# Kernel tuning notes

Hardware: AMD Instinct MI355X
Metric: run time of the kernel (lower is better)

The kernel has to match this reference:

```python
import jax, jax.numpy as jnp
import numpy as np

V = 32000   # vocab
D = 1024    # dim
H = 16      # query heads
HKV = 8     # kv heads (GQA)
DH = D // H # head dim = 64
L = 2       # layers
FF = 3584   # expert hidden dim
E = 8       # experts
K = 2       # top-k
EPS = 1e-5
BASE = 1000000.0
B, S = 1, 2048


def setup_inputs() -> dict:
    key = jax.random.key(0)
    ks = jax.random.split(key, 10)
    s = 0.02
    return {
        "x": jax.random.randint(ks[0], (B, S), 0, V, dtype=jnp.int64) if jax.config.jax_enable_x64 else jax.random.randint(ks[0], (B, S), 0, V),
        "emb": jax.random.normal(ks[1], (V, D), jnp.float32) * s,
        "ln_w": jnp.ones((L, D), jnp.float32),
        "ffln_w": jnp.ones((L, D), jnp.float32),
        "wq": jax.random.normal(ks[2], (L, D, H * DH), jnp.float32) * s,
        "wk": jax.random.normal(ks[3], (L, D, HKV * DH), jnp.float32) * s,
        "wv": jax.random.normal(ks[4], (L, D, HKV * DH), jnp.float32) * s,
        "wo": jax.random.normal(ks[5], (L, H * DH, D), jnp.float32) * s,
        "gate_w": jax.random.normal(ks[6], (L, E, D), jnp.float32) * s,
        "w1": jax.random.normal(ks[7], (L, E, FF, D), jnp.float32) * s,
        "w2": jax.random.normal(ks[8], (L, E, D, FF), jnp.float32) * s,
        "w3": jax.random.normal(ks[9], (L, E, FF, D), jnp.float32) * s,
        "dec_norm_w": jnp.ones((D,), jnp.float32),
    }


def rmsnorm(x, w):
    # LayerNormParameterized(use_mean=False, shift=False) == RMSNorm, pow in fp32
    xf = x.astype(jnp.float32)
    var = jnp.mean(xf * xf, axis=-1, keepdims=True)
    return ((xf * jax.lax.rsqrt(var + EPS)).astype(x.dtype)) * w


def rope(xh, pos):
    # interleaved (complex-pair) rotary embedding, xh: [B, S, h, DH]
    half = DH // 2
    freqs = 1.0 / (BASE ** (jnp.arange(0, half, dtype=jnp.float32) * 2.0 / DH))
    ang = pos[:, None] * freqs[None, :]                       # [S, half]
    cos = jnp.cos(ang)[None, :, None, :]
    sin = jnp.sin(ang)[None, :, None, :]
    x1 = xh[..., 0::2]
    x2 = xh[..., 1::2]
    out = jnp.stack([x1 * cos - x2 * sin, x1 * sin + x2 * cos], axis=-1)
    return out.reshape(xh.shape)


def reference(x, emb, ln_w, ffln_w, wq, wk, wv, wo, gate_w, w1, w2, w3, dec_norm_w):
    h = emb[x]                                                # [B, S, D]
    pos = jnp.arange(S, dtype=jnp.float32)
    causal = jnp.tril(jnp.ones((S, S), bool))[None, None]     # [1,1,S,S]
    scale = 1.0 / np.sqrt(DH).astype(np.float32)
    for i in range(L):
        # --- attention sub-layer ---
        res = h
        xn = rmsnorm(h, ln_w[i])
        q = rope((xn @ wq[i]).reshape(B, S, H, DH), pos)
        k = rope((xn @ wk[i]).reshape(B, S, HKV, DH), pos)
        v = (xn @ wv[i]).reshape(B, S, HKV, DH)
        rep = H // HKV
        k = jnp.repeat(k, rep, axis=2)                        # [B,S,H,DH]
        v = jnp.repeat(v, rep, axis=2)
        scores = jnp.einsum('bqhd,bkhd->bhqk', q, k) * scale
        scores = jnp.where(causal, scores, jnp.float32(-1e9))
        att = jax.nn.softmax(scores, axis=-1)
        o = jnp.einsum('bhqk,bkhd->bqhd', att, v).reshape(B, S, H * DH) @ wo[i]
        h = res + o
        # --- MoE FFN sub-layer ---
        res = h
        xn = rmsnorm(h, ffln_w[i]).reshape(B * S, D)          # [T, D]
        logits = xn @ gate_w[i].T                             # [T, E]
        gates = jax.nn.softmax(logits, axis=-1)
        topw, topi = jax.lax.top_k(gates, K)                  # [T, K]
        topw = topw / jnp.sum(topw, axis=-1, keepdims=True)
        # dense combine weights [T, E] (zero for unselected experts)
        cw = jnp.einsum('tk,tke->te', topw, jax.nn.one_hot(topi, E, dtype=topw.dtype))
        y = jnp.zeros_like(xn)
        for e in range(E):                                    # fixed small expert loop
            ye = (jax.nn.silu(xn @ w1[i, e].T) * (xn @ w3[i, e].T)) @ w2[i, e].T
            y = y + cw[:, e:e + 1] * ye
        h = res + y.reshape(B, S, D)
    return rmsnorm(h, dec_norm_w)
```

## Files before the change

### kernel.cpp

```cpp
#include <hip/hip_runtime.h>

using u16 = unsigned short;
using u32 = unsigned int;

#define TT 2048
#define DM 1024
#define NH 16
#define NKV 8
#define DHD 64
#define FFD 3584
#define NE 8

typedef __bf16 bf16x8 __attribute__((ext_vector_type(8)));
typedef float f32x4 __attribute__((ext_vector_type(4)));

__device__ __forceinline__ u16 f2bf(float x){
  return __builtin_bit_cast(u16, (__bf16)x);
}
__device__ __forceinline__ float bf2f(u16 h){
  return (float)__builtin_bit_cast(__bf16, h);
}
__device__ __forceinline__ f32x4 mfma16(bf16x8 a, bf16x8 b, f32x4 c){
  return __builtin_amdgcn_mfma_f32_16x16x32_bf16(a, b, c, 0, 0, 0);
}
__device__ __forceinline__ uint4 packhi8v(float4 a, float4 b){
  u16 h0=f2bf(a.x),h1=f2bf(a.y),h2=f2bf(a.z),h3=f2bf(a.w);
  u16 h4=f2bf(b.x),h5=f2bf(b.y),h6=f2bf(b.z),h7=f2bf(b.w);
  return make_uint4((u32)h0|((u32)h1<<16),(u32)h2|((u32)h3<<16),
                    (u32)h4|((u32)h5<<16),(u32)h6|((u32)h7<<16));
}
__device__ __forceinline__ uint4 packlo8v(float4 a, float4 b){
  u16 l0=f2bf(a.x-bf2f(f2bf(a.x))),l1=f2bf(a.y-bf2f(f2bf(a.y)));
  u16 l2=f2bf(a.z-bf2f(f2bf(a.z))),l3=f2bf(a.w-bf2f(f2bf(a.w)));
  u16 l4=f2bf(b.x-bf2f(f2bf(b.x))),l5=f2bf(b.y-bf2f(f2bf(b.y)));
  u16 l6=f2bf(b.z-bf2f(f2bf(b.z))),l7=f2bf(b.w-bf2f(f2bf(b.w)));
  return make_uint4((u32)l0|((u32)l1<<16),(u32)l2|((u32)l3<<16),
                    (u32)l4|((u32)l5<<16),(u32)l6|((u32)l7<<16));
}

#define SWZR(r) ((((r)>>1) ^ ((r)>>3)) & 3)
#define SWC(r,c) ((((c) ^ SWZR(r))) * 8)

__device__ __forceinline__ void glds16(const u16* g, u16* l){
  __builtin_amdgcn_global_load_lds(
      (const __attribute__((address_space(1))) void*)g,
      (__attribute__((address_space(3))) void*)l,
      16, 0, 0);
}

__global__ __launch_bounds__(256) void k_embed(const int* __restrict__ x,
    const float* __restrict__ emb, float* __restrict__ h){
  int t = blockIdx.x;
  int d = threadIdx.x * 4;
  float4 v = *reinterpret_cast<const float4*>(emb + (size_t)x[t] * DM + d);
  *reinterpret_cast<float4*>(h + (size_t)t * DM + d) = v;
}

template<int OUTF32>
__global__ __launch_bounds__(256) void k_rmsnorm(const float* __restrict__ in,
    const float* __restrict__ w, u16* __restrict__ oh, u16* __restrict__ ol,
    float* __restrict__ of){
  int t = blockIdx.x;
  int d4 = threadIdx.x * 4;
  float4 xv = *reinterpret_cast<const float4*>(in + (size_t)t * DM + d4);
  float ss = xv.x*xv.x + xv.y*xv.y + xv.z*xv.z + xv.w*xv.w;
#pragma unroll
  for (int m = 1; m < 64; m <<= 1) ss += __shfl_xor(ss, m);
  __shared__ float sred[4];
  if ((threadIdx.x & 63) == 0) sred[threadIdx.x >> 6] = ss;
  __syncthreads();
  float tot = sred[0] + sred[1] + sred[2] + sred[3];
  float r = 1.0f / sqrtf(tot * (1.0f / DM) + 1e-5f);
  float vv[4] = {xv.x, xv.y, xv.z, xv.w};
#pragma unroll
  for (int jj = 0; jj < 4; jj++){
    float xn = (vv[jj] * r) * w[d4 + jj];
    size_t a = (size_t)t * DM + d4 + jj;
    if constexpr (OUTF32){
      of[a] = xn;
    } else {
      u16 hi = f2bf(xn);
      oh[a] = hi;
      ol[a] = f2bf(xn - bf2f(hi));
    }
  }
}

template<int NHD>
__global__ __launch_bounds__(256) void k_rope(const float* __restrict__ in,
    u16* __restrict__ oh, u16* __restrict__ ol){
  int idx = blockIdx.x * 256 + threadIdx.x;
  int j = idx & 31;
  int hd = (idx >> 5) % NHD;
  int s = idx / (32 * NHD);
  size_t base = ((size_t)s * NHD + hd) * 64 + 2 * j;
  float x1 = in[base], x2 = in[base + 1];
  float xe = (float)j * 0.03125f;
  float yf = (float)pow(1.0e6, (double)xe);
  float fr = 1.0f / yf;
  float ang = (float)s * fr;
  double ad = (double)ang;
  float c  = (float)cos(ad);
  float sn = (float)sin(ad);
  float o1 = x1 * c - x2 * sn;
  float o2 = x1 * sn + x2 * c;
  u16 h1 = f2bf(o1), h2 = f2bf(o2);
  oh[base]     = h1; ol[base]     = f2bf(o1 - bf2f(h1));
  oh[base + 1] = h2; ol[base + 1] = f2bf(o2 - bf2f(h2));
}

__global__ __launch_bounds__(256) void k_splitbuf(const float* __restrict__ in,
    u16* __restrict__ oh, u16* __restrict__ ol, int n){
  int i = blockIdx.x * 256 + threadIdx.x;
  if (i < n){
    float x = in[i];
    u16 hi = f2bf(x);
    oh[i] = hi;
    ol[i] = f2bf(x - bf2f(hi));
  }
}

__global__ __launch_bounds__(256) void k_gate(const u16* __restrict__ xh,
    const u16* __restrict__ xl, const float* __restrict__ gw,
    int* __restrict__ topi, float* __restrict__ topw, int* __restrict__ cnt){
  int wv = threadIdx.x >> 6, lane = threadIdx.x & 63;
  int t = blockIdx.x * 4 + wv;
  float x[16];
#pragma unroll
  for (int i = 0; i < 16; i++){
    size_t a = (size_t)t * DM + lane + 64 * i;
    x[i] = bf2f(xh[a]) + bf2f(xl[a]);
  }
  float lgt[8];
#pragma unroll
  for (int e = 0; e < 8; e++){
    float s = 0.f;
#pragma unroll
    for (int i = 0; i < 16; i++) s += x[i] * gw[(size_t)e * DM + lane + 64 * i];
#pragma unroll
    for (int m = 1; m < 64; m <<= 1) s += __shfl_xor(s, m);
    lgt[e] = s;
  }
  float mx = lgt[0];
#pragma unroll
  for (int e = 1; e < 8; e++) mx = fmaxf(mx, lgt[e]);
  float p[8]; float sum = 0.f;
#pragma unroll
  for (int e = 0; e < 8; e++){ p[e] = expf(lgt[e] - mx); sum += p[e]; }
  float g[8];
#pragma unroll
  for (int e = 0; e < 8; e++) g[e] = p[e] / sum;
  int t0 = 0; float b0 = g[0];
#pragma unroll
  for (int e = 1; e < 8; e++) if (g[e] > b0){ b0 = g[e]; t0 = e; }
  int t1 = -1; float b1 = -1.f;
#pragma unroll
  for (int e = 0; e < 8; e++) if (e != t0 && g[e] > b1){ b1 = g[e]; t1 = e; }
  float ssum = b0 + b1;
  float w0 = b0 / ssum, w1 = b1 / ssum;
  if (lane == 0 && t < TT){
    topi[2*t] = t0; topi[2*t+1] = t1;
    topw[2*t] = w0; topw[2*t+1] = w1;
    atomicAdd(&cnt[t0], 1);
    atomicAdd(&cnt[t1], 1);
  }
}

__global__ void k_zero8(int* cnt){ if (threadIdx.x < 8) cnt[threadIdx.x] = 0; }

__global__ void k_scan(const int* __restrict__ cnt, int* __restrict__ offp, int* __restrict__ cur){
  if (threadIdx.x == 0){
    int r = 0;
    for (int e = 0; e < 8; e++){ offp[e] = r; r += cnt[e]; }
  }
  if (threadIdx.x < 8) cur[threadIdx.x] = 0;
}

__global__ __launch_bounds__(256) void k_scatter(const int* __restrict__ topi,
    const float* __restrict__ topw, const int* __restrict__ offp, int* __restrict__ cur,
    int* __restrict__ ftok, float* __restrict__ fwt){
  int t = blockIdx.x * 256 + threadIdx.x;
  if (t < TT){
#pragma unroll
    for (int j = 0; j < 2; j++){
      int e = topi[2*t + j];
      int p = atomicAdd(&cur[e], 1);
      ftok[offp[e] + p] = t;
      fwt[offp[e] + p] = topw[2*t + j];
    }
  }
}

#define GLDSA(BUF, KK) do { \
    glds16(Ah + gaA0 + (KK), (u16*)&Ash[BUF][awr0][0]); \
    glds16(Ah + gaA1 + (KK), (u16*)&Ash[BUF][awr1][0]); \
    if constexpr (SPLIT){ \
      glds16(Al + gaA0 + (KK), (u16*)&Asl[BUF][awr0][0]); \
      glds16(Al + gaA1 + (KK), (u16*)&Asl[BUF][awr1][0]); \
    } \
  } while(0)

#define GPRELOADB(KK) do { \
    if constexpr (BLAYOUT == 0){ \
      const float* bp_ = Bw + (size_t)(n0 + br0) * K + (KK) + cb8; \
      pB0 = *reinterpret_cast<const float4*>(bp_); \
      pB1 = *reinterpret_cast<const float4*>(bp_ + 4); \
      if constexpr (TN == 128){ \
        const float* bp2_ = Bw + (size_t)(n0 + br1) * K + (KK) + cb8; \
        pB2 = *reinterpret_cast<const float4*>(bp2_); \
        pB3 = *reinterpret_cast<const float4*>(bp2_ + 4); \
      } \
      if constexpr (DUAL){ \
        const float* bq_ = B3w + (size_t)(n0 + br0) * K + (KK) + cb8; \
        pB2 = *reinterpret_cast<const float4*>(bq_); \
        pB3 = *reinterpret_cast<const float4*>(bq_ + 4); \
      } \
    } else { \
      pB0 = *reinterpret_cast<const float4*>(Bw + (size_t)((KK) + kk1) * Nq + n0 + nn1); \
      pB1 = *reinterpret_cast<const float4*>(Bw + (size_t)((KK) + 16 + kk1) * Nq + n0 + nn1); \
    } \
  } while(0)

#define GSTOREB() do { \
    if constexpr (BLAYOUT == 0){ \
      *reinterpret_cast<uint4*>(&Bh1[br0][swB0]) = packhi8v(pB0, pB1); \
      if constexpr (SPLIT) *reinterpret_cast<uint4*>(&Bl1[br0][swB0]) = packlo8v(pB0, pB1); \
      if constexpr (TN == 128){ \
        *reinterpret_cast<uint4*>(&Bh1[br1][swB1]) = packhi8v(pB2, pB3); \
        if constexpr (SPLIT) *reinterpret_cast<uint4*>(&Bl1[br1][swB1]) = packlo8v(pB2, pB3); \
      } \
      if constexpr (DUAL){ \
        *reinterpret_cast<uint4*>(&Bh3[br0][swB0]) = packhi8v(pB2, pB3); \
        if constexpr (SPLIT) *reinterpret_cast<uint4*>(&Bl3[br0][swB0]) = packlo8v(pB2, pB3); \
      } \
    } else { \
      const float* q0 = reinterpret_cast<const float*>(&pB0); \
      const float* q1 = reinterpret_cast<const float*>(&pB1); \
      const int ch0 = kk1 >> 3, off0 = kk1 & 7; \
      _Pragma("unroll") \
      for (int j = 0; j < 4; j++){ \
        int row = nn1 + j; \
        int c0 = SWC(row, ch0) + off0; \
        int c1 = SWC(row, ch0 + 2) + off0; \
        u16 h0 = f2bf(q0[j]); \
        Bh1[row][c0] = h0; \
        if constexpr (SPLIT) Bl1[row][c0] = f2bf(q0[j] - bf2f(h0)); \
        u16 h1 = f2bf(q1[j]); \
        Bh1[row][c1] = h1; \
        if constexpr (SPLIT) Bl1[row][c1] = f2bf(q1[j] - bf2f(h1)); \
      } \
    } \
  } while(0)

#define MFMA_PHASE(CURB) do { \
    bf16x8 af[4], afl[4]; \
    _Pragma("unroll") \
    for (int m = 0; m < 4; m++){ \
      int Ra = wr*64 + m*16 + lr; \
      int sa = SWC(Ra, lg); \
      af[m] = *reinterpret_cast<const bf16x8*>(&Ash[CURB][Ra][sa]); \
      if constexpr (SPLIT) \
        afl[m] = *reinterpret_cast<const bf16x8*>(&Asl[CURB][Ra][sa]); \
    } \
    _Pragma("unroll") \
    for (int n = 0; n < NF; n++){ \
      int Rb = wc*(TN/2) + n*16 + lr; \
      int sb = SWC(Rb, lg); \
      bf16x8 b1 = *reinterpret_cast<const bf16x8*>(&Bh1[Rb][sb]); \
      _Pragma("unroll") \
      for (int m = 0; m < 4; m++) acc[m][n] = mfma16(af[m], b1, acc[m][n]); \
      if constexpr (SPLIT){ \
        bf16x8 bl = *reinterpret_cast<const bf16x8*>(&Bl1[Rb][sb]); \
        _Pragma("unroll") \
        for (int m = 0; m < 4; m++){ \
          acc[m][n] = mfma16(af[m], bl, acc[m][n]); \
          acc[m][n] = mfma16(afl[m], b1, acc[m][n]); \
        } \
      } \
      if constexpr (DUAL){ \
        bf16x8 b3 = *reinterpret_cast<const bf16x8*>(&Bh3[Rb][sb]); \
        _Pragma("unroll") \
        for (int m = 0; m < 4; m++) acc3[m][n] = mfma16(af[m], b3, acc3[m][n]); \
        if constexpr (SPLIT){ \
          bf16x8 b3l = *reinterpret_cast<const bf16x8*>(&Bl3[Rb][sb]); \
          _Pragma("unroll") \
          for (int m = 0; m < 4; m++){ \
            acc3[m][n] = mfma16(af[m], b3l, acc3[m][n]); \
            acc3[m][n] = mfma16(afl[m], b3, acc3[m][n]); \
          } \
        } \
      } \
    } \
  } while(0)

template<int BLAYOUT, int EPI, int SPLIT, int DUAL, int TN, int KS>
__global__ __launch_bounds__(256) void k_gemm(
    const u16* __restrict__ Ah, const u16* __restrict__ Al,
    const float* __restrict__ Bw, const float* __restrict__ B3w,
    const float* __restrict__ Bw2, const float* __restrict__ Bw3,
    size_t strideB, int N, int K,
    float* __restrict__ Cf, int ldc,
    float* __restrict__ Cf2, float* __restrict__ Cf3,
    u16* __restrict__ Ch, u16* __restrict__ Cl,
    const int* __restrict__ cntp, const int* __restrict__ offp,
    const int* __restrict__ ftok, const float* __restrict__ fwt)
{
  static_assert(!(DUAL && TN != 64), "DUAL uses TN=64");
  static_assert(!(BLAYOUT == 1 && TN != 64), "BLAYOUT=1 uses TN=64");
  int cnt = TT, off = 0, ks = 0;
  if constexpr (EPI == 2 || EPI == 3){
    int e = blockIdx.z / KS;
    ks = blockIdx.z % KS;
    cnt = cntp[e]; off = offp[e];
    if ((int)blockIdx.y * 128 >= cnt) return;
    Bw += (size_t)e * strideB;
    if constexpr (DUAL) B3w += (size_t)e * strideB;
  } else if constexpr (KS > 1){
    ks = blockIdx.z;
  }
  __shared__ u16 Ash[2][128][32];
  __shared__ u16 Asl[SPLIT ? 2 : 1][SPLIT ? 128 : 1][32];
  __shared__ u16 Bh1[TN][32];
  __shared__ u16 Bl1[SPLIT ? TN : 1][32];
  __shared__ u16 Bh3[DUAL ? TN : 1][32];
  __shared__ u16 Bl3[(DUAL && SPLIT) ? TN : 1][32];

  const int tid = threadIdx.x;
  const int m0 = blockIdx.y * 128;

  int n0, Nq = N, ldq = ldc;
  float* Cq = Cf;
  if constexpr (EPI == 4){
    int bx = blockIdx.x;
    if (bx < 16){       n0 = bx * 64;        Nq = 1024; ldq = 1024; Cq = Cf;  }
    else if (bx < 24){  n0 = (bx - 16) * 64; Nq = 512;  ldq = 512;  Cq = Cf2; Bw = Bw2; }
    else {              n0 = (bx - 24) * 64; Nq = 512;  ldq = 512;  Cq = Cf3; Bw = Bw3; }
  } else {
    n0 = blockIdx.x * TN;
  }

  const int wid = tid >> 6, lane = tid & 63;
  const int wr = wid >> 1, wc = wid & 1;
  const int lr = lane & 15, lg = lane >> 4;
  constexpr int NF = TN / 32;

  const int awr0 = wid * 32;
  const int awr1 = wid * 32 + 16;
  const int rA0 = awr0 + (lane >> 2);
  const int rA1 = awr1 + (lane >> 2);
  const int cA0 = (lane & 3) ^ SWZR(rA0);
  const int cA1 = (lane & 3) ^ SWZR(rA1);
  int grA0, grA1;
  {
    int g0 = m0 + rA0, g1 = m0 + rA1;
    if constexpr (EPI == 2){
      grA0 = ftok[off + (g0 < cnt ? g0 : cnt - 1)];
      grA1 = ftok[off + (g1 < cnt ? g1 : cnt - 1)];
    } else if constexpr (EPI == 3){
      grA0 = off + (g0 < cnt ? g0 : cnt - 1);
      grA1 = off + (g1 < cnt ? g1 : cnt - 1);
    } else {
      grA0 = g0; grA1 = g1;
    }
  }
  const size_t gaA0 = (size_t)grA0 * K + cA0 * 8;
  const size_t gaA1 = (size_t)grA1 * K + cA1 * 8;

  const int br0 = tid >> 2;
  const int br1 = br0 + 64;
  const int cb8 = (tid & 3) * 8;
  const int swB0 = SWC(br0, tid & 3), swB1 = SWC(br1, tid & 3);
  const int kk1 = tid >> 4;
  const int nn1 = (tid & 15) * 4;

  f32x4 acc[4][NF];
  f32x4 acc3[DUAL ? 4 : 1][NF];
#pragma unroll
  for (int m = 0; m < 4; m++)
#pragma unroll
    for (int n = 0; n < NF; n++){
      acc[m][n] = f32x4{0.f,0.f,0.f,0.f};
      if constexpr (DUAL) acc3[m][n] = f32x4{0.f,0.f,0.f,0.f};
    }

  float4 pB0{}, pB1{}, pB2{}, pB3{};

  const int kbeg = ks * (K / KS);
  const int kend = kbeg + (K / KS);

  GLDSA(0, kbeg);
  GPRELOADB(kbeg);
  int cur = 0;
  for (int k0 = kbeg; k0 < kend; k0 += 32){
    GSTOREB();
    asm volatile("s_waitcnt vmcnt(0) lgkmcnt(0)" ::: "memory");
    __builtin_amdgcn_s_barrier();
    if (k0 + 32 < kend){
      GLDSA(cur ^ 1, k0 + 32);
      GPRELOADB(k0 + 32);
    }
    MFMA_PHASE(cur);
    __builtin_amdgcn_s_barrier();
    cur ^= 1;
  }

#pragma unroll
  for (int m = 0; m < 4; m++)
#pragma unroll
    for (int n = 0; n < NF; n++)
#pragma unroll
      for (int r = 0; r < 4; r++){
        int row = m0 + wr*64 + m*16 + lg*4 + r;
        int col = n0 + wc*(TN/2) + n*16 + lr;
        float v = acc[m][n][r];
        if constexpr (EPI == 0){
          Cf[(size_t)row * ldc + col] = v;
        } else if constexpr (EPI == 1){
          if constexpr (KS > 1) atomicAdd(&Cf[(size_t)row * ldc + col], v);
          else                  Cf[(size_t)row * ldc + col] += v;
        } else if constexpr (EPI == 2){
          if (row < cnt){
            float a3 = acc3[m][n][r];
            float s = v / (1.0f + expf(-v));
            float y = s * a3;
            u16 hi = f2bf(y);
            size_t oa = (size_t)(off + row) * ldc + col;
            Ch[oa] = hi;
            Cl[oa] = f2bf(y - bf2f(hi));
          }
        } else if constexpr (EPI == 3){
          if (row < cnt){
            int tok = ftok[off + row];
            float wgt = fwt[off + row];
            atomicAdd(&Cf[(size_t)tok * ldc + col], wgt * v);
          }
        } else {
          if constexpr (KS > 1) atomicAdd(&Cq[(size_t)row * ldq + col], v);
          else                  Cq[(size_t)row * ldq + col] = v;
        }
      }
}

__global__ __launch_bounds__(256) void k_attn(
    const u16* __restrict__ qh, const u16* __restrict__ ql,
    const u16* __restrict__ kh, const u16* __restrict__ kl,
    const u16* __restrict__ vh, const u16* __restrict__ vl,
    u16* __restrict__ aoh, u16* __restrict__ aol)
{
  const int h  = blockIdx.y;
  const int q0 = blockIdx.x * 64;
  const int hk = h >> 1;
  const int tid = threadIdx.x;
  const int wv = tid >> 6, lane = tid & 63;
  const int lr = lane & 15, lg = lane >> 4;
  const int qw0 = q0 + wv * 16;

  __shared__ u16 Khs[32][72], Kls[32][72];
  __shared__ u16 Vhs[64][40], Vls[64][40];
  __shared__ u16 Phs[4][16][40], Pls[4][16][40];

  bf16x8 qfh[2], qfl[2];
#pragma unroll
  for (int dc = 0; dc < 2; dc++){
    size_t qa = ((size_t)(qw0 + lr) * NH + h) * 64 + dc*32 + lg*8;
    qfh[dc] = *reinterpret_cast<const bf16x8*>(qh + qa);
    qfl[dc] = *reinterpret_cast<const bf16x8*>(ql + qa);
  }
  f32x4 oacc[4];
  float mrun[4], lrun[4];
#pragma unroll
  for (int r = 0; r < 4; r++){ mrun[r] = -1e30f; lrun[r] = 0.f; }
#pragma unroll
  for (int g = 0; g < 4; g++) oacc[g] = f32x4{0.f,0.f,0.f,0.f};

  const int nt = q0 / 32 + 2;
  for (int kt = 0; kt < nt; kt++){
    int kg = kt * 32;
    {
      int kk = tid >> 3, c8 = (tid & 7) * 8;
      size_t ka = ((size_t)(kg + kk) * NKV + hk) * 64 + c8;
      *reinterpret_cast<uint4*>(&Khs[kk][c8]) = *reinterpret_cast<const uint4*>(kh + ka);
      *reinterpret_cast<uint4*>(&Kls[kk][c8]) = *reinterpret_cast<const uint4*>(kl + ka);
      uint4 v1 = *reinterpret_cast<const uint4*>(vh + ka);
      uint4 v2 = *reinterpret_cast<const uint4*>(vl + ka);
      const u16* p1 = reinterpret_cast<const u16*>(&v1);
      const u16* p2 = reinterpret_cast<const u16*>(&v2);
#pragma unroll
      for (int j = 0; j < 8; j++){ Vhs[c8 + j][kk] = p1[j]; Vls[c8 + j][kk] = p2[j]; }
    }
    __syncthreads();

    f32x4 sc[2];
    sc[0] = f32x4{0.f,0.f,0.f,0.f};
    sc[1] = f32x4{0.f,0.f,0.f,0.f};
#pragma unroll
    for (int c = 0; c < 2; c++){
#pragma unroll
      for (int dc = 0; dc < 2; dc++){
        bf16x8 bh = *reinterpret_cast<const bf16x8*>(&Khs[c*16 + lr][dc*32 + lg*8]);
        bf16x8 bl = *reinterpret_cast<const bf16x8*>(&Kls[c*16 + lr][dc*32 + lg*8]);
        sc[c] = mfma16(qfh[dc], bh, sc[c]);
        sc[c] = mfma16(qfh[dc], bl, sc[c]);
        sc[c] = mfma16(qfl[dc], bh, sc[c]);
      }
    }
    float pnew[2][4], corr[4];
#pragma unroll
    for (int r = 0; r < 4; r++){
      int row = qw0 + lg*4 + r;
      float s0 = (kg + lr      <= row) ? sc[0][r] * 0.125f : -1e30f;
      float s1 = (kg + 16 + lr <= row) ? sc[1][r] * 0.125f : -1e30f;
      float tm = fmaxf(s0, s1);
#pragma unroll
      for (int m = 1; m < 16; m <<= 1) tm = fmaxf(tm, __shfl_xor(tm, m));
      float mnew = fmaxf(mrun[r], tm);
      corr[r] = expf(mrun[r] - mnew);
      float p0 = expf(s0 - mnew);
      float p1 = expf(s1 - mnew);
      pnew[0][r] = p0; pnew[1][r] = p1;
      float sm = p0 + p1;
#pragma unroll
      for (int m = 1; m < 16; m <<= 1) sm += __shfl_xor(sm, m);
      lrun[r] = lrun[r] * corr[r] + sm;
      mrun[r] = mnew;
    }
#pragma unroll
    for (int g = 0; g < 4; g++){
      f32x4 t = oacc[g];
#pragma unroll
      for (int r = 0; r < 4; r++) t[r] *= corr[r];
      oacc[g] = t;
    }
#pragma unroll
    for (int c = 0; c < 2; c++)
#pragma unroll
      for (int r = 0; r < 4; r++){
        float p = pnew[c][r];
        u16 hi = f2bf(p);
        Phs[wv][lg*4 + r][c*16 + lr] = hi;
        Pls[wv][lg*4 + r][c*16 + lr] = f2bf(p - bf2f(hi));
      }
    asm volatile("s_waitcnt lgkmcnt(0)" ::: "memory");
    __builtin_amdgcn_sched_barrier(0);
    bf16x8 pah = *reinterpret_cast<const bf16x8*>(&Phs[wv][lr][lg*8]);
    bf16x8 pal = *reinterpret_cast<const bf16x8*>(&Pls[wv][lr][lg*8]);
#pragma unroll
    for (int g = 0; g < 4; g++){
      bf16x8 vb1 = *reinterpret_cast<const bf16x8*>(&Vhs[g*16 + lr][lg*8]);
      bf16x8 vb2 = *reinterpret_cast<const bf16x8*>(&Vls[g*16 + lr][lg*8]);
      oacc[g] = mfma16(pah, vb1, oacc[g]);
      oacc[g] = mfma16(pah, vb2, oacc[g]);
      oacc[g] = mfma16(pal, vb1, oacc[g]);
    }
    __syncthreads();
  }
#pragma unroll
  for (int g = 0; g < 4; g++)
#pragma unroll
    for (int r = 0; r < 4; r++){
      int row = qw0 + lg*4 + r;
      float v = oacc[g][r] / lrun[r];
      u16 hi = f2bf(v);
      size_t oa = ((size_t)row * NH + h) * 64 + g*16 + lr;
      aoh[oa] = hi;
      aol[oa] = f2bf(v - bf2f(hi));
    }
}

extern "C" void kernel_launch(void* const* d_in, const int* in_sizes, int n_in,
                              void* d_out, int out_size, void* d_ws, size_t ws_size,
                              hipStream_t stream){
  const int*   x     = (const int*)d_in[0];
  const float* emb   = (const float*)d_in[1];
  const float* lnw   = (const float*)d_in[2];
  const float* fflnw = (const float*)d_in[3];
  const float* wq    = (const float*)d_in[4];
  const float* wk    = (const float*)d_in[5];
  const float* wvp   = (const float*)d_in[6];
  const float* wo    = (const float*)d_in[7];
  const float* gw    = (const float*)d_in[8];
  const float* w1    = (const float*)d_in[9];
  const float* w2    = (const float*)d_in[10];
  const float* w3    = (const float*)d_in[11];
  const float* dnw   = (const float*)d_in[12];
  float* out = (float*)d_out;

  char* p = (char*)d_ws;
  auto alloc = [&](size_t bytes)->char*{
    char* r = p; p += (bytes + 255) & ~(size_t)255; return r;
  };
  float* h    = (float*)alloc((size_t)TT * DM * 4);
  float* qbuf = (float*)alloc((size_t)TT * 1024 * 4);
  float* kbuf = (float*)alloc((size_t)TT * 512 * 4);
  float* vbuf = (float*)alloc((size_t)TT * 512 * 4);
  u16* xnh = (u16*)alloc((size_t)TT * DM * 2);
  u16* xnl = (u16*)alloc((size_t)TT * DM * 2);
  u16* qhb = (u16*)alloc((size_t)TT * 1024 * 2);
  u16* qlb = (u16*)alloc((size_t)TT * 1024 * 2);
  u16* khb = (u16*)alloc((size_t)TT * 512 * 2);
  u16* klb = (u16*)alloc((size_t)TT * 512 * 2);
  u16* vhb = (u16*)alloc((size_t)TT * 512 * 2);
  u16* vlb = (u16*)alloc((size_t)TT * 512 * 2);
  u16* aoh = (u16*)alloc((size_t)TT * 1024 * 2);
  u16* aol = (u16*)alloc((size_t)TT * 1024 * 2);
  u16* acth = (u16*)alloc((size_t)2 * TT * FFD * 2);
  u16* actl = (u16*)alloc((size_t)2 * TT * FFD * 2);
  int*   topi = (int*)alloc((size_t)2 * TT * 4);
  float* topw = (float*)alloc((size_t)2 * TT * 4);
  int* cnt  = (int*)alloc(64);
  int* offe = (int*)alloc(64);
  int* cur  = (int*)alloc(64);
  int*   ftok = (int*)alloc((size_t)2 * TT * 4);
  float* fwt  = (float*)alloc((size_t)2 * TT * 4);

  k_embed<<<TT, 256, 0, stream>>>(x, emb, h);

  for (int i = 0; i < 2; i++){
    const float* wq_i = wq + (size_t)i * DM * 1024;
    const float* wk_i = wk + (size_t)i * DM * 512;
    const float* wv_i = wvp + (size_t)i * DM * 512;
    const float* wo_i = wo + (size_t)i * 1024 * DM;
    const float* w1_i = w1 + (size_t)i * NE * FFD * DM;
    const float* w2_i = w2 + (size_t)i * NE * DM * FFD;
    const float* w3_i = w3 + (size_t)i * NE * FFD * DM;

    k_rmsnorm<0><<<TT, 256, 0, stream>>>(h, lnw + i * DM, xnh, xnl, nullptr);

    hipMemsetAsync(qbuf, 0, (size_t)TT * 1024 * 4, stream);
    hipMemsetAsync(kbuf, 0, (size_t)TT * 512 * 4, stream);
    hipMemsetAsync(vbuf, 0, (size_t)TT * 512 * 4, stream);
    k_gemm<1,4,1,0,64,2><<<dim3(32,16,2), 256, 0, stream>>>(xnh, xnl,
        wq_i, nullptr, wk_i, wv_i, 0, 1024, DM,
        qbuf, 1024, kbuf, vbuf, nullptr, nullptr, nullptr, nullptr, nullptr, nullptr);

    k_rope<16><<<4096, 256, 0, stream>>>(qbuf, qhb, qlb);
    k_rope<8><<<2048, 256, 0, stream>>>(kbuf, khb, klb);
    k_splitbuf<<<4096, 256, 0, stream>>>(vbuf, vhb, vlb, TT * 512);

    k_attn<<<dim3(32,16,1), 256, 0, stream>>>(qhb, qlb, khb, klb, vhb, vlb, aoh, aol);

    k_gemm<1,1,1,0,64,2><<<dim3(16,16,2), 256, 0, stream>>>(aoh, aol,
        wo_i, nullptr, nullptr, nullptr, 0, DM, 1024,
        h, DM, nullptr, nullptr, nullptr, nullptr, nullptr, nullptr, nullptr, nullptr);

    k_rmsnorm<0><<<TT, 256, 0, stream>>>(h, fflnw + i * DM, xnh, xnl, nullptr);

    k_zero8<<<1, 64, 0, stream>>>(cnt);
    k_gate<<<TT/4, 256, 0, stream>>>(xnh, xnl, gw + (size_t)i * NE * DM, topi, topw, cnt);
    k_scan<<<1, 64, 0, stream>>>(cnt, offe, cur);
    k_scatter<<<8, 256, 0, stream>>>(topi, topw, offe, cur, ftok, fwt);

    if (i == 0){
      k_gemm<0,2,1,1,64,1><<<dim3(FFD/64,16,8), 256, 0, stream>>>(xnh, xnl,
          w1_i, w3_i, nullptr, nullptr, (size_t)FFD * DM, FFD, DM,
          nullptr, FFD, nullptr, nullptr, acth, actl, cnt, offe, ftok, fwt);
      k_gemm<0,3,1,0,128,4><<<dim3(DM/128,16,32), 256, 0, stream>>>(acth, actl,
          w2_i, nullptr, nullptr, nullptr, (size_t)DM * FFD, DM, FFD,
          h, DM, nullptr, nullptr, nullptr, nullptr, cnt, offe, ftok, fwt);
    } else {
      k_gemm<0,2,0,1,64,1><<<dim3(FFD/64,16,8), 256, 0, stream>>>(xnh, xnl,
          w1_i, w3_i, nullptr, nullptr, (size_t)FFD * DM, FFD, DM,
          nullptr, FFD, nullptr, nullptr, acth, actl, cnt, offe, ftok, fwt);
      k_gemm<0,3,0,0,128,4><<<dim3(DM/128,16,32), 256, 0, stream>>>(acth, actl,
          w2_i, nullptr, nullptr, nullptr, (size_t)DM * FFD, DM, FFD,
          h, DM, nullptr, nullptr, nullptr, nullptr, cnt, offe, ftok, fwt);
    }
  }

  k_rmsnorm<1><<<TT, 256, 0, stream>>>(h, dnw, nullptr, nullptr, out);
}
```

Measured before the change: 1.499 ms.

## Load row-major B fragments straight into registers, bypassing shared memory

For the row-major weight layout, each wave now loads its fp32 B values directly from global memory into registers already arranged in the MFMA operand layout. It converts them to bf16 hi/lo in registers and prefetches the next k-slice while the MFMAs run. This removes the shared-memory store and reload of B and one barrier per k-step, and raises wave priority around the MFMA blocks. In exchange, waves that share a column block fetch the same B data redundantly, and the per-lane global loads are strided by rows rather than coalesced.

```diff
diff --git a/kernel.cpp b/kernel.cpp
--- a/kernel.cpp
+++ b/kernel.cpp
@@ -36,6 +36,20 @@
   u16 l6=f2bf(b.z-bf2f(f2bf(b.z))),l7=f2bf(b.w-bf2f(f2bf(b.w)));
   return make_uint4((u32)l0|((u32)l1<<16),(u32)l2|((u32)l3<<16),
                     (u32)l4|((u32)l5<<16),(u32)l6|((u32)l7<<16));
+}
+__device__ __forceinline__ bf16x8 cvthi8(float4 a, float4 b){
+  bf16x8 r;
+  r[0]=(__bf16)a.x; r[1]=(__bf16)a.y; r[2]=(__bf16)a.z; r[3]=(__bf16)a.w;
+  r[4]=(__bf16)b.x; r[5]=(__bf16)b.y; r[6]=(__bf16)b.z; r[7]=(__bf16)b.w;
+  return r;
+}
+__device__ __forceinline__ bf16x8 cvtlo8(float4 a, float4 b){
+  bf16x8 r;
+  r[0]=(__bf16)(a.x-(float)(__bf16)a.x); r[1]=(__bf16)(a.y-(float)(__bf16)a.y);
+  r[2]=(__bf16)(a.z-(float)(__bf16)a.z); r[3]=(__bf16)(a.w-(float)(__bf16)a.w);
+  r[4]=(__bf16)(b.x-(float)(__bf16)b.x); r[5]=(__bf16)(b.y-(float)(__bf16)b.y);
+  r[6]=(__bf16)(b.z-(float)(__bf16)b.z); r[7]=(__bf16)(b.w-(float)(__bf16)b.w);
+  return r;
 }
 
 #define SWZR(r) ((((r)>>1) ^ ((r)>>3)) & 3)
@@ -200,59 +214,95 @@
     } \
   } while(0)
 
-#define GPRELOADB(KK) do { \
-    if constexpr (BLAYOUT == 0){ \
-      const float* bp_ = Bw + (size_t)(n0 + br0) * K + (KK) + cb8; \
-      pB0 = *reinterpret_cast<const float4*>(bp_); \
-      pB1 = *reinterpret_cast<const float4*>(bp_ + 4); \
-      if constexpr (TN == 128){ \
-        const float* bp2_ = Bw + (size_t)(n0 + br1) * K + (KK) + cb8; \
-        pB2 = *reinterpret_cast<const float4*>(bp2_); \
-        pB3 = *reinterpret_cast<const float4*>(bp2_ + 4); \
+#define BLOADALL(KK) do { \
+    pBr[0] = *reinterpret_cast<const float4*>(bs0 + (KK)); \
+    pBr[1] = *reinterpret_cast<const float4*>(bs0 + (KK) + 4); \
+    pBr[2] = *reinterpret_cast<const float4*>(bs1 + (KK)); \
+    pBr[3] = *reinterpret_cast<const float4*>(bs1 + (KK) + 4); \
+    pBr[4] = *reinterpret_cast<const float4*>(bs2 + (KK)); \
+    pBr[5] = *reinterpret_cast<const float4*>(bs2 + (KK) + 4); \
+    pBr[6] = *reinterpret_cast<const float4*>(bs3 + (KK)); \
+    pBr[7] = *reinterpret_cast<const float4*>(bs3 + (KK) + 4); \
+  } while(0)
+
+#define NB_SINGLE(NB, I0, I1, BP) do { \
+    bf16x8 f1h = cvthi8(pBr[I0], pBr[I1]); \
+    bf16x8 f1l{}; \
+    if constexpr (SPLIT) f1l = cvtlo8(pBr[I0], pBr[I1]); \
+    if (more){ \
+      pBr[I0] = *reinterpret_cast<const float4*>(BP + k0 + 32); \
+      pBr[I1] = *reinterpret_cast<const float4*>(BP + k0 + 36); \
+    } \
+    __builtin_amdgcn_s_setprio(1); \
+    _Pragma("unroll") \
+    for (int m = 0; m < 4; m++) acc[m][NB] = mfma16(af[m], f1h, acc[m][NB]); \
+    if constexpr (SPLIT){ \
+      _Pragma("unroll") \
+      for (int m = 0; m < 4; m++){ \
+        acc[m][NB] = mfma16(af[m], f1l, acc[m][NB]); \
+        acc[m][NB] = mfma16(afl[m], f1h, acc[m][NB]); \
       } \
-      if constexpr (DUAL){ \
-        const float* bq_ = B3w + (size_t)(n0 + br0) * K + (KK) + cb8; \
-        pB2 = *reinterpret_cast<const float4*>(bq_); \
-        pB3 = *reinterpret_cast<const float4*>(bq_ + 4); \
+    } \
+    __builtin_amdgcn_s_setprio(0); \
+  } while(0)
+
+#define NB_DUAL(NB, I0, I1, J0, J1, BP1, BP3) do { \
+    bf16x8 f1h = cvthi8(pBr[I0], pBr[I1]); \
+    bf16x8 f3h = cvthi8(pBr[J0], pBr[J1]); \
+    bf16x8 f1l{}, f3l{}; \
+    if constexpr (SPLIT){ f1l = cvtlo8(pBr[I0], pBr[I1]); f3l = cvtlo8(pBr[J0], pBr[J1]); } \
+    if (more){ \
+      pBr[I0] = *reinterpret_cast<const float4*>(BP1 + k0 + 32); \
+      pBr[I1] = *reinterpret_cast<const float4*>(BP1 + k0 + 36); \
+      pBr[J0] = *reinterpret_cast<const float4*>(BP3 + k0 + 32); \
+      pBr[J1] = *reinterpret_cast<const float4*>(BP3 + k0 + 36); \
+    } \
+    __builtin_amdgcn_s_setprio(1); \
+    _Pragma("unroll") \
+    for (int m = 0; m < 4; m++) acc[m][NB] = mfma16(af[m], f1h, acc[m][NB]); \
+    if constexpr (SPLIT){ \
+      _Pragma("unroll") \
+      for (int m = 0; m < 4; m++){ \
+        acc[m][NB] = mfma16(af[m], f1l, acc[m][NB]); \
+        acc[m][NB] = mfma16(afl[m], f1h, acc[m][NB]); \
       } \
-    } else { \
-      pB0 = *reinterpret_cast<const float4*>(Bw + (size_t)((KK) + kk1) * Nq + n0 + nn1); \
-      pB1 = *reinterpret_cast<const float4*>(Bw + (size_t)((KK) + 16 + kk1) * Nq + n0 + nn1); \
-    } \
+    } \
+    _Pragma("unroll") \
+    for (int m = 0; m < 4; m++) acc3[m][NB] = mfma16(af[m], f3h, acc3[m][NB]); \
+    if constexpr (SPLIT){ \
+      _Pragma("unroll") \
+      for (int m = 0; m < 4; m++){ \
+        acc3[m][NB] = mfma16(af[m], f3l, acc3[m][NB]); \
+        acc3[m][NB] = mfma16(afl[m], f3h, acc3[m][NB]); \
+      } \
+    } \
+    __builtin_amdgcn_s_setprio(0); \
   } while(0)
 
-#define GSTOREB() do { \
-    if constexpr (BLAYOUT == 0){ \
-      *reinterpret_cast<uint4*>(&Bh1[br0][swB0]) = packhi8v(pB0, pB1); \
-      if constexpr (SPLIT) *reinterpret_cast<uint4*>(&Bl1[br0][swB0]) = packlo8v(pB0, pB1); \
-      if constexpr (TN == 128){ \
-        *reinterpret_cast<uint4*>(&Bh1[br1][swB1]) = packhi8v(pB2, pB3); \
-        if constexpr (SPLIT) *reinterpret_cast<uint4*>(&Bl1[br1][swB1]) = packlo8v(pB2, pB3); \
-      } \
-      if constexpr (DUAL){ \
-        *reinterpret_cast<uint4*>(&Bh3[br0][swB0]) = packhi8v(pB2, pB3); \
-        if constexpr (SPLIT) *reinterpret_cast<uint4*>(&Bl3[br0][swB0]) = packlo8v(pB2, pB3); \
-      } \
-    } else { \
-      const float* q0 = reinterpret_cast<const float*>(&pB0); \
-      const float* q1 = reinterpret_cast<const float*>(&pB1); \
-      const int ch0 = kk1 >> 3, off0 = kk1 & 7; \
-      _Pragma("unroll") \
-      for (int j = 0; j < 4; j++){ \
-        int row = nn1 + j; \
-        int c0 = SWC(row, ch0) + off0; \
-        int c1 = SWC(row, ch0 + 2) + off0; \
-        u16 h0 = f2bf(q0[j]); \
-        Bh1[row][c0] = h0; \
-        if constexpr (SPLIT) Bl1[row][c0] = f2bf(q0[j] - bf2f(h0)); \
-        u16 h1 = f2bf(q1[j]); \
-        Bh1[row][c1] = h1; \
-        if constexpr (SPLIT) Bl1[row][c1] = f2bf(q1[j] - bf2f(h1)); \
-      } \
-    } \
+#define GPRELOADB1(KK) do { \
+    pB0 = *reinterpret_cast<const float4*>(Bw + (size_t)((KK) + kk1) * Nq + n0 + nn1); \
+    pB1 = *reinterpret_cast<const float4*>(Bw + (size_t)((KK) + 16 + kk1) * Nq + n0 + nn1); \
   } while(0)
 
-#define MFMA_PHASE(CURB) do { \
+#define GSTOREB1() do { \
+    const float* q0 = reinterpret_cast<const float*>(&pB0); \
+    const float* q1 = reinterpret_cast<const float*>(&pB1); \
+    const int ch0 = kk1 >> 3, off0 = kk1 & 7; \
+    _Pragma("unroll") \
+    for (int j = 0; j < 4; j++){ \
+      int row = nn1 + j; \
+      int c0 = SWC(row, ch0) + off0; \
+      int c1 = SWC(row, ch0 + 2) + off0; \
+      u16 h0 = f2bf(q0[j]); \
+      Bh1[row][c0] = h0; \
+      if constexpr (SPLIT) Bl1[row][c0] = f2bf(q0[j] - bf2f(h0)); \
+      u16 h1 = f2bf(q1[j]); \
+      Bh1[row][c1] = h1; \
+      if constexpr (SPLIT) Bl1[row][c1] = f2bf(q1[j] - bf2f(h1)); \
+    } \
+  } while(0)
+
+#define MFMA_PHASE1(CURB) do { \
     bf16x8 af[4], afl[4]; \
     _Pragma("unroll") \
     for (int m = 0; m < 4; m++){ \
@@ -262,6 +312,7 @@
       if constexpr (SPLIT) \
         afl[m] = *reinterpret_cast<const bf16x8*>(&Asl[CURB][Ra][sa]); \
     } \
+    __builtin_amdgcn_s_setprio(1); \
     _Pragma("unroll") \
     for (int n = 0; n < NF; n++){ \
       int Rb = wc*(TN/2) + n*16 + lr; \
@@ -277,20 +328,8 @@
           acc[m][n] = mfma16(afl[m], b1, acc[m][n]); \
         } \
       } \
-      if constexpr (DUAL){ \
-        bf16x8 b3 = *reinterpret_cast<const bf16x8*>(&Bh3[Rb][sb]); \
-        _Pragma("unroll") \
-        for (int m = 0; m < 4; m++) acc3[m][n] = mfma16(af[m], b3, acc3[m][n]); \
-        if constexpr (SPLIT){ \
-          bf16x8 b3l = *reinterpret_cast<const bf16x8*>(&Bl3[Rb][sb]); \
-          _Pragma("unroll") \
-          for (int m = 0; m < 4; m++){ \
-            acc3[m][n] = mfma16(af[m], b3l, acc3[m][n]); \
-            acc3[m][n] = mfma16(afl[m], b3, acc3[m][n]); \
-          } \
-        } \
-      } \
-    } \
+    } \
+    __builtin_amdgcn_s_setprio(0); \
   } while(0)
 
 template<int BLAYOUT, int EPI, int SPLIT, int DUAL, int TN, int KS>
@@ -307,6 +346,8 @@
 {
   static_assert(!(DUAL && TN != 64), "DUAL uses TN=64");
   static_assert(!(BLAYOUT == 1 && TN != 64), "BLAYOUT=1 uses TN=64");
+  constexpr int NF = TN / 32;
+  static_assert(BLAYOUT == 1 || NF * (DUAL ? 2 : 1) == 4, "BREG path needs 4 B sources");
   int cnt = TT, off = 0, ks = 0;
   if constexpr (EPI == 2 || EPI == 3){
     int e = blockIdx.z / KS;
@@ -320,10 +361,8 @@
   }
   __shared__ u16 Ash[2][128][32];
   __shared__ u16 Asl[SPLIT ? 2 : 1][SPLIT ? 128 : 1][32];
-  __shared__ u16 Bh1[TN][32];
-  __shared__ u16 Bl1[SPLIT ? TN : 1][32];
-  __shared__ u16 Bh3[DUAL ? TN : 1][32];
-  __shared__ u16 Bl3[(DUAL && SPLIT) ? TN : 1][32];
+  __shared__ u16 Bh1[BLAYOUT == 1 ? TN : 1][32];
+  __shared__ u16 Bl1[(BLAYOUT == 1 && SPLIT) ? TN : 1][32];
 
   const int tid = threadIdx.x;
   const int m0 = blockIdx.y * 128;
@@ -342,7 +381,6 @@
   const int wid = tid >> 6, lane = tid & 63;
   const int wr = wid >> 1, wc = wid & 1;
   const int lr = lane & 15, lg = lane >> 4;
-  constexpr int NF = TN / 32;
 
   const int awr0 = wid * 32;
   const int awr1 = wid * 32 + 16;
@@ -366,13 +404,6 @@
   const size_t gaA0 = (size_t)grA0 * K + cA0 * 8;
   const size_t gaA1 = (size_t)grA1 * K + cA1 * 8;
 
-  const int br0 = tid >> 2;
-  const int br1 = br0 + 64;
-  const int cb8 = (tid & 3) * 8;
-  const int swB0 = SWC(br0, tid & 3), swB1 = SWC(br1, tid & 3);
-  const int kk1 = tid >> 4;
-  const int nn1 = (tid & 15) * 4;
-
   f32x4 acc[4][NF];
   f32x4 acc3[DUAL ? 4 : 1][NF];
 #pragma unroll
@@ -383,25 +414,71 @@
       if constexpr (DUAL) acc3[m][n] = f32x4{0.f,0.f,0.f,0.f};
     }
 
-  float4 pB0{}, pB1{}, pB2{}, pB3{};
-
   const int kbeg = ks * (K / KS);
   const int kend = kbeg + (K / KS);
 
-  GLDSA(0, kbeg);
-  GPRELOADB(kbeg);
-  int cur = 0;
-  for (int k0 = kbeg; k0 < kend; k0 += 32){
-    GSTOREB();
-    asm volatile("s_waitcnt vmcnt(0) lgkmcnt(0)" ::: "memory");
-    __builtin_amdgcn_s_barrier();
-    if (k0 + 32 < kend){
-      GLDSA(cur ^ 1, k0 + 32);
-      GPRELOADB(k0 + 32);
-    }
-    MFMA_PHASE(cur);
-    __builtin_amdgcn_s_barrier();
-    cur ^= 1;
+  if constexpr (BLAYOUT == 0){
+    const float *bs0, *bs1, *bs2, *bs3;
+    if constexpr (DUAL){
+      bs0 = Bw  + (size_t)(n0 + wc*32 + lr) * K + lg*8;
+      bs1 = Bw  + (size_t)(n0 + wc*32 + 16 + lr) * K + lg*8;
+      bs2 = B3w + (size_t)(n0 + wc*32 + lr) * K + lg*8;
+      bs3 = B3w + (size_t)(n0 + wc*32 + 16 + lr) * K + lg*8;
+    } else {
+      bs0 = Bw + (size_t)(n0 + wc*64 + lr) * K + lg*8;
+      bs1 = Bw + (size_t)(n0 + wc*64 + 16 + lr) * K + lg*8;
+      bs2 = Bw + (size_t)(n0 + wc*64 + 32 + lr) * K + lg*8;
+      bs3 = Bw + (size_t)(n0 + wc*64 + 48 + lr) * K + lg*8;
+    }
+    float4 pBr[8];
+    GLDSA(0, kbeg);
+    BLOADALL(kbeg);
+    int cur = 0;
+    for (int k0 = kbeg; k0 < kend; k0 += 32){
+      asm volatile("s_waitcnt vmcnt(0)" ::: "memory");
+      __builtin_amdgcn_s_barrier();
+      __builtin_amdgcn_sched_barrier(0);
+      const bool more = (k0 + 32 < kend);
+      if (more) GLDSA(cur ^ 1, k0 + 32);
+      bf16x8 af[4], afl[4];
+#pragma unroll
+      for (int m = 0; m < 4; m++){
+        int Ra = wr*64 + m*16 + lr;
+        int sa = SWC(Ra, lg);
+        af[m] = *reinterpret_cast<const bf16x8*>(&Ash[cur][Ra][sa]);
+        if constexpr (SPLIT)
+          afl[m] = *reinterpret_cast<const bf16x8*>(&Asl[cur][Ra][sa]);
+      }
+      if constexpr (DUAL){
+        NB_DUAL(0, 0, 1, 4, 5, bs0, bs2);
+        NB_DUAL(1, 2, 3, 6, 7, bs1, bs3);
+      } else {
+        NB_SINGLE(0, 0, 1, bs0);
+        NB_SINGLE(1, 2, 3, bs1);
+        NB_SINGLE(2, 4, 5, bs2);
+        NB_SINGLE(3, 6, 7, bs3);
+      }
+      cur ^= 1;
+    }
+  } else {
+    const int kk1 = tid >> 4;
+    const int nn1 = (tid & 15) * 4;
+    float4 pB0{}, pB1{};
+    GLDSA(0, kbeg);
+    GPRELOADB1(kbeg);
+    int cur = 0;
+    for (int k0 = kbeg; k0 < kend; k0 += 32){
+      GSTOREB1();
+      asm volatile("s_waitcnt vmcnt(0) lgkmcnt(0)" ::: "memory");
+      __builtin_amdgcn_s_barrier();
+      if (k0 + 32 < kend){
+        GLDSA(cur ^ 1, k0 + 32);
+        GPRELOADB1(k0 + 32);
+      }
+      MFMA_PHASE1(cur);
+      __builtin_amdgcn_s_barrier();
+      cur ^= 1;
+    }
   }
 
 #pragma unroll
```

Measured after the change: 1.993 ms. +33.0%, slower.
